# Optimization experiments

Measured on AMD Instinct MI355X. Metric: run time of the kernel, lower is better.

Reference implementation:

```python
import jax, jax.numpy as jnp
import numpy as np

# canonical 3x3 lattice offsets, (dy,dx) pairs in row-major kernel order (mmcv offset layout)
CANON = jnp.array([[-1,-1],[-1,0],[-1,1],[0,-1],[0,0],[0,1],[1,-1],[1,0],[1,1]], dtype=jnp.float32)  # (9,2)
BASE_DILATION = 1.0

def conv3x3(x, w, b):
    # x: (B,Cin,H,W), w: (Cout,Cin,3,3), stride 1, pad 1
    y = jax.lax.conv_general_dilated(x, w, window_strides=(1, 1), padding=((1, 1), (1, 1)),
                                     dimension_numbers=('NCHW', 'OIHW', 'NCHW'))
    return y + b[None, :, None, None]

def _bilinear_sample(img, ys, xs):
    # img: (Cg,H,W); ys,xs: (9,H,W) float sample coords. Zero outside bounds (per-corner).
    Cg, Hn, Wn = img.shape
    y0 = jnp.floor(ys); x0 = jnp.floor(xs)
    wy = ys - y0; wx = xs - x0
    y0i = y0.astype(jnp.int32); x0i = x0.astype(jnp.int32)
    flat = img.reshape(Cg, Hn * Wn)
    def corner(yi, xi, w):
        valid = (yi >= 0) & (yi < Hn) & (xi >= 0) & (xi < Wn)
        idx = jnp.clip(yi, 0, Hn - 1) * Wn + jnp.clip(xi, 0, Wn - 1)
        v = jnp.take(flat, idx.reshape(-1), axis=1).reshape((Cg,) + yi.shape)
        return v * (w * valid.astype(img.dtype))[None]
    return (corner(y0i, x0i, (1 - wy) * (1 - wx)) + corner(y0i, x0i + 1, (1 - wy) * wx)
            + corner(y0i + 1, x0i, wy * (1 - wx)) + corner(y0i + 1, x0i + 1, wy * wx))  # (Cg,9,H,W)

def setup_inputs() -> dict:
    key = jax.random.key(0)
    ks = jax.random.split(key, 7)
    B, C, H, W = 4, 256, 64, 64
    O, dg = 256, 1
    x = jax.random.normal(ks[0], (B, C, H, W), dtype=jnp.float32)
    weight = jax.random.normal(ks[1], (O, C, 3, 3), dtype=jnp.float32) * (2.0 / (C * 9)) ** 0.5
    bias = jnp.zeros((O,), dtype=jnp.float32)
    w_scale = jax.random.normal(ks[2], (dg, C, 3, 3), dtype=jnp.float32) * 0.01
    b_scale = jnp.full((dg,), 0.5, dtype=jnp.float32)
    w_mask = jax.random.normal(ks[3], (dg * 9, C, 3, 3), dtype=jnp.float32) * 0.01
    b_mask = jnp.zeros((dg * 9,), dtype=jnp.float32)
    return {"x": x, "weight": weight, "bias": bias, "w_scale": w_scale,
            "b_scale": b_scale, "w_mask": w_mask, "b_mask": b_mask}

def reference(x, weight, bias, w_scale, b_scale, w_mask, b_mask):
    B, C, H, W = x.shape
    dg = w_scale.shape[0]
    O = weight.shape[0]
    Cg = C // dg
    # radial scale s(x) >= 0 (use_zero_dilation=False): (B,dg,H,W)
    scale = jax.nn.relu(conv3x3(x, w_scale, b_scale)) * BASE_DILATION
    # modulation mask: (B,dg,9,H,W)
    mask = jax.nn.sigmoid(conv3x3(x, w_mask, b_mask)).reshape(B, dg, 9, H, W)
    # learned offset = scale * canonical lattice: (B,dg,9,2,H,W)
    off = scale[:, :, None, None, :, :] * CANON[None, None, :, :, None, None]
    # sampling coords: p0 (out pos * stride - pad) + kernel offset * dilation(=1) + learned offset
    base_y = jnp.arange(H, dtype=x.dtype)[None, None, None, :, None] - 1.0  # pad=1
    base_x = jnp.arange(W, dtype=x.dtype)[None, None, None, None, :] - 1.0
    ys = base_y + CANON[:, 0][None, None, :, None, None] + off[:, :, :, 0]  # (B,dg,9,H,W)
    xs = base_x + CANON[:, 1][None, None, :, None, None] + off[:, :, :, 1]
    xg = x.reshape(B, dg, Cg, H, W)
    sampled = jax.vmap(jax.vmap(_bilinear_sample))(xg, ys, xs)  # (B,dg,Cg,9,H,W)
    val = (sampled * mask[:, :, None]).reshape(B, C, 9, H, W)
    out = jnp.einsum('bckhw,ock->bohw', val, weight.reshape(O, C, 9))
    return out + bias[None, :, None, None]
```

## Files before the change

kernel.cpp:

```cpp
#include <hip/hip_runtime.h>
#include <stdint.h>

#define B_ 4
#define C_ 256
#define H_ 64
#define W_ 64
#define O_ 256
#define K_ 2304
#define HW 4096
#define NPIX 16384

typedef unsigned short u16;
typedef __attribute__((ext_vector_type(8))) short bf16x8;
typedef __attribute__((ext_vector_type(4))) float f32x4;

__device__ __forceinline__ u16 f2bf(float f) {
    union { float f; uint32_t u; } v; v.f = f;
    uint32_t u = v.u;
    return (u16)((u + 0x7FFFu + ((u >> 16) & 1u)) >> 16);
}
__device__ __forceinline__ float bf2f(u16 u) {
    union { uint32_t u; float f; } v; v.u = ((uint32_t)u) << 16;
    return v.f;
}

__global__ __launch_bounds__(512) void k_scale_mask(
    const float* __restrict__ x, const float* __restrict__ w_scale,
    const float* __restrict__ w_mask, float* __restrict__ part,
    u16* __restrict__ xT)
{
    __shared__ f32x4 wsm4[64 * 24];
    __shared__ float red[10 * 8 * 64];
    __shared__ u16 xt[64 * 72];

    int bh = blockIdx.x;
    int cg = blockIdx.y;
    int b = bh >> 6, h = bh & 63;
    int tid = threadIdx.x;
    int w = tid & 63;
    int wv = tid >> 6;

    float* wsm = (float*)wsm4;
    for (int i = tid; i < 64 * 96; i += 512) {
        int cl = i / 96, r = i % 96;
        int c = cg * 64 + cl;
        float v = 0.f;
        if (r < 9) {
            v = w_scale[c * 9 + r];
        } else if (r < 90) {
            int j = (r - 9) / 9, k = (r - 9) % 9;
            v = w_mask[((size_t)(j * C_ + c)) * 9 + k];
        }
        wsm[i] = v;
    }
    __syncthreads();

    float acc[10];
#pragma unroll
    for (int o = 0; o < 10; ++o) acc[o] = 0.f;

    const float* xb = x + (size_t)b * (C_ * HW);
#pragma unroll 1
    for (int cc = 0; cc < 8; ++cc) {
        int cl = wv * 8 + cc;
        const float* xp = xb + (cg * 64 + cl) * HW;
        float xv[9];
#pragma unroll
        for (int dy = -1; dy <= 1; ++dy) {
            int hh = h + dy;
            bool hv = (hh >= 0) && (hh < 64);
#pragma unroll
            for (int dx = -1; dx <= 1; ++dx) {
                int ww = w + dx;
                bool vld = hv && (ww >= 0) && (ww < 64);
                xv[(dy + 1) * 3 + (dx + 1)] = vld ? xp[hh * 64 + ww] : 0.f;
            }
        }
        xt[w * 72 + cl] = f2bf(xv[4]);

        const f32x4* wr4 = wsm4 + cl * 24;
        f32x4 wq[23];
#pragma unroll
        for (int q = 0; q < 23; ++q) wq[q] = wr4[q];

#pragma unroll
        for (int k = 0; k < 9; ++k)
            acc[0] = fmaf(xv[k], wq[k >> 2][k & 3], acc[0]);
#pragma unroll
        for (int j = 0; j < 9; ++j) {
#pragma unroll
            for (int k = 0; k < 9; ++k) {
                int r = 9 + j * 9 + k;
                acc[1 + j] = fmaf(xv[k], wq[r >> 2][r & 3], acc[1 + j]);
            }
        }
    }

#pragma unroll
    for (int o = 0; o < 10; ++o) red[(o * 8 + wv) * 64 + w] = acc[o];
    __syncthreads();

    {
        int ww = tid >> 3, c8 = (tid & 7) * 8;
        uint4 v = *(const uint4*)(xt + ww * 72 + c8);
        *(uint4*)(xT + ((size_t)(bh * 64 + ww)) * 256 + cg * 64 + c8) = v;
    }

    if (tid < 64) {
        float* pout = part + ((size_t)(cg * 256 + bh) * 10) * 64 + tid;
#pragma unroll
        for (int o = 0; o < 10; ++o) {
            float t = 0.f;
#pragma unroll
            for (int g = 0; g < 8; ++g) t += red[(o * 8 + g) * 64 + tid];
            pout[o * 64] = t;
        }
    }
}

__global__ __launch_bounds__(256) void k_finalize(
    const float* __restrict__ part, const float* __restrict__ b_scale,
    const float* __restrict__ b_mask, float* __restrict__ scale_o,
    float* __restrict__ mask_o)
{
    int tid = threadIdx.x;
    int bh = blockIdx.x * 4 + (tid >> 6);
    int w = tid & 63;
    int b = bh >> 6, h = bh & 63;
#pragma unroll
    for (int o = 0; o < 10; ++o) {
        float t = 0.f;
#pragma unroll
        for (int cg = 0; cg < 4; ++cg)
            t += part[((size_t)(cg * 256 + bh) * 10 + o) * 64 + w];
        if (o == 0) {
            float s = t + b_scale[0];
            scale_o[bh * 64 + w] = s > 0.f ? s : 0.f;
        } else {
            float m = t + b_mask[o - 1];
            mask_o[(b * 9 + (o - 1)) * HW + h * 64 + w] = 1.f / (1.f + expf(-m));
        }
    }
}

__global__ __launch_bounds__(256) void k_pack_w(const float* __restrict__ wgt,
                                                u16* __restrict__ wbf)
{
    int k = blockIdx.x, o = blockIdx.y, c = threadIdx.x;
    wbf[(size_t)o * K_ + k * 256 + c] = f2bf(wgt[(size_t)o * K_ + c * 9 + k]);
}

__global__ __launch_bounds__(256) void k_val2(
    const u16* __restrict__ xT, const float* __restrict__ scale_i,
    const float* __restrict__ mask_i, u16* __restrict__ val)
{
    int wv = threadIdx.x >> 6, lane = threadIdx.x & 63;
    int p = blockIdx.x * 4 + wv;
    int b = p >> 12, hw = p & 4095;
    int h = hw >> 6, w = hw & 63;
    float d = 1.f + scale_i[p];
    const u16* xb = xT + ((size_t)(b << 12)) * 256;
    u16* vout = val + (size_t)p * K_;
    int c0 = lane * 4;

#pragma unroll 3
    for (int k = 0; k < 9; ++k) {
        int dy = k / 3 - 1, dx = k % 3 - 1;
        float ysf = (float)(h - 1) + (float)dy * d;
        float xsf = (float)(w - 1) + (float)dx * d;
        float y0f = floorf(ysf), x0f = floorf(xsf);
        float wy = ysf - y0f, wx = xsf - x0f;
        int y0 = (int)y0f, x0 = (int)x0f;
        int y1 = y0 + 1, x1 = x0 + 1;
        float vy0 = (y0 >= 0 && y0 < 64) ? 1.f : 0.f;
        float vy1 = (y1 >= 0 && y1 < 64) ? 1.f : 0.f;
        float vx0 = (x0 >= 0 && x0 < 64) ? 1.f : 0.f;
        float vx1 = (x1 >= 0 && x1 < 64) ? 1.f : 0.f;

        float m = mask_i[(b * 9 + k) * HW + hw];
        float w00 = (1.f - wy) * (1.f - wx) * m * vy0 * vx0;
        float w01 = (1.f - wy) * wx * m * vy0 * vx1;
        float w10 = wy * (1.f - wx) * m * vy1 * vx0;
        float w11 = wy * wx * m * vy1 * vx1;

        int cy0 = min(max(y0, 0), 63), cy1 = min(max(y1, 0), 63);
        int cx0 = min(max(x0, 0), 63), cx1 = min(max(x1, 0), 63);

        const u16* p00 = xb + (size_t)(cy0 * 64 + cx0) * 256 + c0;
        const u16* p01 = xb + (size_t)(cy0 * 64 + cx1) * 256 + c0;
        const u16* p10 = xb + (size_t)(cy1 * 64 + cx0) * 256 + c0;
        const u16* p11 = xb + (size_t)(cy1 * 64 + cx1) * 256 + c0;
        ushort4 v00 = *(const ushort4*)p00;
        ushort4 v01 = *(const ushort4*)p01;
        ushort4 v10 = *(const ushort4*)p10;
        ushort4 v11 = *(const ushort4*)p11;

        float rx = fmaf(w00, bf2f(v00.x), fmaf(w01, bf2f(v01.x), fmaf(w10, bf2f(v10.x), w11 * bf2f(v11.x))));
        float ry = fmaf(w00, bf2f(v00.y), fmaf(w01, bf2f(v01.y), fmaf(w10, bf2f(v10.y), w11 * bf2f(v11.y))));
        float rz = fmaf(w00, bf2f(v00.z), fmaf(w01, bf2f(v01.z), fmaf(w10, bf2f(v10.z), w11 * bf2f(v11.z))));
        float rw = fmaf(w00, bf2f(v00.w), fmaf(w01, bf2f(v01.w), fmaf(w10, bf2f(v10.w), w11 * bf2f(v11.w))));

        ushort4 pk;
        pk.x = f2bf(rx); pk.y = f2bf(ry); pk.z = f2bf(rz); pk.w = f2bf(rw);
        *(ushort4*)(vout + k * 256 + c0) = pk;
    }
}

__global__ __launch_bounds__(256, 2) void k_gemm(
    const u16* __restrict__ wbf, const u16* __restrict__ val,
    const float* __restrict__ bias, float* __restrict__ out)
{
    __shared__ u16 As[128 * 72];
    __shared__ u16 Bs[64 * 72];
    int tid = threadIdx.x;
    int lane = tid & 63;
    int wv = tid >> 6;
    int wm = wv >> 1, wn = wv & 1;
    int n0 = blockIdx.x * 64;
    int m0 = blockIdx.y * 128;
    int l15 = lane & 15, l4 = lane >> 4;

    f32x4 acc[4][2];
#pragma unroll
    for (int i = 0; i < 4; ++i)
#pragma unroll
        for (int j = 0; j < 2; ++j) acc[i][j] = (f32x4){0.f, 0.f, 0.f, 0.f};

    int rr = tid >> 3;
    int c8 = (tid & 7) * 8;

    const u16* ap = wbf + (size_t)(m0 + rr) * K_ + c8;
    const u16* bp = val + (size_t)(n0 + rr) * K_ + c8;

    uint4 ra0 = *(const uint4*)(ap);
    uint4 ra1 = *(const uint4*)(ap + (size_t)32 * K_);
    uint4 ra2 = *(const uint4*)(ap + (size_t)64 * K_);
    uint4 ra3 = *(const uint4*)(ap + (size_t)96 * K_);
    uint4 rb0 = *(const uint4*)(bp);
    uint4 rb1 = *(const uint4*)(bp + (size_t)32 * K_);

    for (int k0 = 0; k0 < K_; k0 += 64) {
        __syncthreads();
        *(uint4*)(As + rr * 72 + c8) = ra0;
        *(uint4*)(As + (rr + 32) * 72 + c8) = ra1;
        *(uint4*)(As + (rr + 64) * 72 + c8) = ra2;
        *(uint4*)(As + (rr + 96) * 72 + c8) = ra3;
        *(uint4*)(Bs + rr * 72 + c8) = rb0;
        *(uint4*)(Bs + (rr + 32) * 72 + c8) = rb1;
        __syncthreads();

        int kn = k0 + 64;
        if (kn < K_) {
            ra0 = *(const uint4*)(ap + kn);
            ra1 = *(const uint4*)(ap + (size_t)32 * K_ + kn);
            ra2 = *(const uint4*)(ap + (size_t)64 * K_ + kn);
            ra3 = *(const uint4*)(ap + (size_t)96 * K_ + kn);
            rb0 = *(const uint4*)(bp + kn);
            rb1 = *(const uint4*)(bp + (size_t)32 * K_ + kn);
        }

#pragma unroll
        for (int kk = 0; kk < 2; ++kk) {
            bf16x8 af[4], bg[2];
#pragma unroll
            for (int i = 0; i < 4; ++i)
                af[i] = *(const bf16x8*)(As + (wm * 64 + i * 16 + l15) * 72 + kk * 32 + l4 * 8);
#pragma unroll
            for (int j = 0; j < 2; ++j)
                bg[j] = *(const bf16x8*)(Bs + (wn * 32 + j * 16 + l15) * 72 + kk * 32 + l4 * 8);
#pragma unroll
            for (int i = 0; i < 4; ++i)
#pragma unroll
                for (int j = 0; j < 2; ++j)
                    acc[i][j] = __builtin_amdgcn_mfma_f32_16x16x32_bf16(af[i], bg[j], acc[i][j], 0, 0, 0);
        }
    }

    int bidx = n0 >> 12;
    int hwbase = n0 & 4095;
#pragma unroll
    for (int i = 0; i < 4; ++i)
#pragma unroll
        for (int j = 0; j < 2; ++j)
#pragma unroll
            for (int t = 0; t < 4; ++t) {
                int row = wm * 64 + i * 16 + l4 * 4 + t;
                int col = wn * 32 + j * 16 + l15;
                int o = m0 + row;
                out[((size_t)(bidx * O_ + o)) * HW + hwbase + col] = acc[i][j][t] + bias[o];
            }
}

extern "C" void kernel_launch(void* const* d_in, const int* in_sizes, int n_in,
                              void* d_out, int out_size, void* d_ws, size_t ws_size,
                              hipStream_t stream) {
    const float* x       = (const float*)d_in[0];
    const float* weight  = (const float*)d_in[1];
    const float* bias    = (const float*)d_in[2];
    const float* w_scale = (const float*)d_in[3];
    const float* b_scale = (const float*)d_in[4];
    const float* w_mask  = (const float*)d_in[5];
    const float* b_mask  = (const float*)d_in[6];
    float* out = (float*)d_out;

    char* ws = (char*)d_ws;
    float* scale_ws = (float*)ws;
    float* mask_ws  = (float*)(ws + 65536);
    u16*   wbf      = (u16*)(ws + 65536 + 589824);
    u16*   val      = (u16*)(ws + 65536 + 589824 + 1179648);
    u16*   xT       = (u16*)(ws + 65536 + 589824 + 1179648 + 75497472);
    float* part_ws  = (float*)val;

    k_scale_mask<<<dim3(B_ * H_, 4), 512, 0, stream>>>(x, w_scale, w_mask, part_ws, xT);
    k_finalize<<<dim3(64), 256, 0, stream>>>(part_ws, b_scale, b_mask, scale_ws, mask_ws);
    k_pack_w<<<dim3(9, O_), 256, 0, stream>>>(weight, wbf);
    k_val2<<<dim3(NPIX / 4), 256, 0, stream>>>(xT, scale_ws, mask_ws, val);
    k_gemm<<<dim3(NPIX / 64, O_ / 128), 256, 0, stream>>>(wbf, val, bias, out);
}
```

Baseline: 171.2 us.

## Fuse deformable bilinear sampling into the GEMM B-tile load

Removes the separate k_val2 kernel that materialized the sampled/masked im2col matrix (about 75MB bf16) and instead computes the bilinear samples directly while loading each B tile in the GEMM. This avoids writing and re-reading the large intermediate buffer. In exchange, sampling is recomputed for each of the two M-blocks. The register prefetch of the next tile is dropped, so global load latency is no longer overlapped with the MFMA work.

```diff
diff --git a/kernel.cpp b/kernel.cpp
--- a/kernel.cpp
+++ b/kernel.cpp
@@ -19,9 +19,11 @@
     uint32_t u = v.u;
     return (u16)((u + 0x7FFFu + ((u >> 16) & 1u)) >> 16);
 }
-__device__ __forceinline__ float bf2f(u16 u) {
-    union { uint32_t u; float f; } v; v.u = ((uint32_t)u) << 16;
-    return v.f;
+__device__ __forceinline__ float bflo(uint32_t u) {
+    union { uint32_t u; float f; } v; v.u = u << 16; return v.f;
+}
+__device__ __forceinline__ float bfhi(uint32_t u) {
+    union { uint32_t u; float f; } v; v.u = u & 0xffff0000u; return v.f;
 }
 
 __global__ __launch_bounds__(512) void k_scale_mask(
@@ -150,64 +152,58 @@
     wbf[(size_t)o * K_ + k * 256 + c] = f2bf(wgt[(size_t)o * K_ + c * 9 + k]);
 }
 
-__global__ __launch_bounds__(256) void k_val2(
-    const u16* __restrict__ xT, const float* __restrict__ scale_i,
-    const float* __restrict__ mask_i, u16* __restrict__ val)
-{
-    int wv = threadIdx.x >> 6, lane = threadIdx.x & 63;
-    int p = blockIdx.x * 4 + wv;
-    int b = p >> 12, hw = p & 4095;
-    int h = hw >> 6, w = hw & 63;
-    float d = 1.f + scale_i[p];
-    const u16* xb = xT + ((size_t)(b << 12)) * 256;
-    u16* vout = val + (size_t)p * K_;
-    int c0 = lane * 4;
-
-#pragma unroll 3
-    for (int k = 0; k < 9; ++k) {
-        int dy = k / 3 - 1, dx = k % 3 - 1;
-        float ysf = (float)(h - 1) + (float)dy * d;
-        float xsf = (float)(w - 1) + (float)dx * d;
-        float y0f = floorf(ysf), x0f = floorf(xsf);
-        float wy = ysf - y0f, wx = xsf - x0f;
-        int y0 = (int)y0f, x0 = (int)x0f;
-        int y1 = y0 + 1, x1 = x0 + 1;
-        float vy0 = (y0 >= 0 && y0 < 64) ? 1.f : 0.f;
-        float vy1 = (y1 >= 0 && y1 < 64) ? 1.f : 0.f;
-        float vx0 = (x0 >= 0 && x0 < 64) ? 1.f : 0.f;
-        float vx1 = (x1 >= 0 && x1 < 64) ? 1.f : 0.f;
-
-        float m = mask_i[(b * 9 + k) * HW + hw];
-        float w00 = (1.f - wy) * (1.f - wx) * m * vy0 * vx0;
-        float w01 = (1.f - wy) * wx * m * vy0 * vx1;
-        float w10 = wy * (1.f - wx) * m * vy1 * vx0;
-        float w11 = wy * wx * m * vy1 * vx1;
-
-        int cy0 = min(max(y0, 0), 63), cy1 = min(max(y1, 0), 63);
-        int cx0 = min(max(x0, 0), 63), cx1 = min(max(x1, 0), 63);
-
-        const u16* p00 = xb + (size_t)(cy0 * 64 + cx0) * 256 + c0;
-        const u16* p01 = xb + (size_t)(cy0 * 64 + cx1) * 256 + c0;
-        const u16* p10 = xb + (size_t)(cy1 * 64 + cx0) * 256 + c0;
-        const u16* p11 = xb + (size_t)(cy1 * 64 + cx1) * 256 + c0;
-        ushort4 v00 = *(const ushort4*)p00;
-        ushort4 v01 = *(const ushort4*)p01;
-        ushort4 v10 = *(const ushort4*)p10;
-        ushort4 v11 = *(const ushort4*)p11;
-
-        float rx = fmaf(w00, bf2f(v00.x), fmaf(w01, bf2f(v01.x), fmaf(w10, bf2f(v10.x), w11 * bf2f(v11.x))));
-        float ry = fmaf(w00, bf2f(v00.y), fmaf(w01, bf2f(v01.y), fmaf(w10, bf2f(v10.y), w11 * bf2f(v11.y))));
-        float rz = fmaf(w00, bf2f(v00.z), fmaf(w01, bf2f(v01.z), fmaf(w10, bf2f(v10.z), w11 * bf2f(v11.z))));
-        float rw = fmaf(w00, bf2f(v00.w), fmaf(w01, bf2f(v01.w), fmaf(w10, bf2f(v10.w), w11 * bf2f(v11.w))));
-
-        ushort4 pk;
-        pk.x = f2bf(rx); pk.y = f2bf(ry); pk.z = f2bf(rz); pk.w = f2bf(rw);
-        *(ushort4*)(vout + k * 256 + c0) = pk;
-    }
-}
-
-__global__ __launch_bounds__(256, 2) void k_gemm(
-    const u16* __restrict__ wbf, const u16* __restrict__ val,
+__device__ __forceinline__ uint4 bilin8(const u16* __restrict__ xb, int cb,
+    int i00, int i01, int i10, int i11,
+    float w00, float w01, float w10, float w11)
+{
+    uint4 u00 = *(const uint4*)(xb + (size_t)i00 * 256 + cb);
+    uint4 u01 = *(const uint4*)(xb + (size_t)i01 * 256 + cb);
+    uint4 u10 = *(const uint4*)(xb + (size_t)i10 * 256 + cb);
+    uint4 u11 = *(const uint4*)(xb + (size_t)i11 * 256 + cb);
+    const uint32_t* p00 = &u00.x;
+    const uint32_t* p01 = &u01.x;
+    const uint32_t* p10 = &u10.x;
+    const uint32_t* p11 = &u11.x;
+    uint4 r;
+    uint32_t* pr = &r.x;
+#pragma unroll
+    for (int i = 0; i < 4; ++i) {
+        float lo = fmaf(w00, bflo(p00[i]), fmaf(w01, bflo(p01[i]),
+                   fmaf(w10, bflo(p10[i]), w11 * bflo(p11[i]))));
+        float hi = fmaf(w00, bfhi(p00[i]), fmaf(w01, bfhi(p01[i]),
+                   fmaf(w10, bfhi(p10[i]), w11 * bfhi(p11[i]))));
+        pr[i] = (uint32_t)f2bf(lo) | ((uint32_t)f2bf(hi) << 16);
+    }
+    return r;
+}
+
+__device__ __forceinline__ void tapcoord(int h, int w, float d, float mm,
+    int dy, int dx, float& w00, float& w01, float& w10, float& w11,
+    int& i00, int& i01, int& i10, int& i11)
+{
+    float ys = (float)(h - 1) + (float)dy * d;
+    float xs = (float)(w - 1) + (float)dx * d;
+    float y0f = floorf(ys), x0f = floorf(xs);
+    float wy = ys - y0f, wx = xs - x0f;
+    int y0 = (int)y0f, x0 = (int)x0f;
+    int y1 = y0 + 1, x1 = x0 + 1;
+    float vy0 = (y0 >= 0 && y0 < 64) ? 1.f : 0.f;
+    float vy1 = (y1 >= 0 && y1 < 64) ? 1.f : 0.f;
+    float vx0 = (x0 >= 0 && x0 < 64) ? 1.f : 0.f;
+    float vx1 = (x1 >= 0 && x1 < 64) ? 1.f : 0.f;
+    w00 = (1.f - wy) * (1.f - wx) * mm * vy0 * vx0;
+    w01 = (1.f - wy) * wx * mm * vy0 * vx1;
+    w10 = wy * (1.f - wx) * mm * vy1 * vx0;
+    w11 = wy * wx * mm * vy1 * vx1;
+    int cy0 = min(max(y0, 0), 63), cy1 = min(max(y1, 0), 63);
+    int cx0 = min(max(x0, 0), 63), cx1 = min(max(x1, 0), 63);
+    i00 = cy0 * 64 + cx0; i01 = cy0 * 64 + cx1;
+    i10 = cy1 * 64 + cx0; i11 = cy1 * 64 + cx1;
+}
+
+__global__ __launch_bounds__(256, 2) void k_gemm_fused(
+    const u16* __restrict__ wbf, const u16* __restrict__ xT,
+    const float* __restrict__ scale_i, const float* __restrict__ mask_i,
     const float* __restrict__ bias, float* __restrict__ out)
 {
     __shared__ u16 As[128 * 72];
@@ -229,35 +225,50 @@
     int rr = tid >> 3;
     int c8 = (tid & 7) * 8;
 
+    int b = n0 >> 12;
+    int hw0 = (n0 & 4095) + rr;
+    int hw1 = hw0 + 32;
+    int h0 = hw0 >> 6, w0c = hw0 & 63;
+    int h1 = hw1 >> 6, w1c = hw1 & 63;
+    float d0 = 1.f + scale_i[n0 + rr];
+    float d1 = 1.f + scale_i[n0 + rr + 32];
+    const u16* xb = xT + (((size_t)b) << 12) * 256;
+    const float* mrow = mask_i + (size_t)b * 9 * HW;
+
     const u16* ap = wbf + (size_t)(m0 + rr) * K_ + c8;
-    const u16* bp = val + (size_t)(n0 + rr) * K_ + c8;
-
-    uint4 ra0 = *(const uint4*)(ap);
-    uint4 ra1 = *(const uint4*)(ap + (size_t)32 * K_);
-    uint4 ra2 = *(const uint4*)(ap + (size_t)64 * K_);
-    uint4 ra3 = *(const uint4*)(ap + (size_t)96 * K_);
-    uint4 rb0 = *(const uint4*)(bp);
-    uint4 rb1 = *(const uint4*)(bp + (size_t)32 * K_);
+
+    float w00a, w01a, w10a, w11a, w00b, w01b, w10b, w11b;
+    int i00a, i01a, i10a, i11a, i00b, i01b, i10b, i11b;
 
     for (int k0 = 0; k0 < K_; k0 += 64) {
+        int tap = k0 >> 8;
+        if ((k0 & 255) == 0) {
+            int dy = tap / 3 - 1, dx = tap % 3 - 1;
+            float mm0 = mrow[tap * HW + hw0];
+            float mm1 = mrow[tap * HW + hw1];
+            tapcoord(h0, w0c, d0, mm0, dy, dx, w00a, w01a, w10a, w11a,
+                     i00a, i01a, i10a, i11a);
+            tapcoord(h1, w1c, d1, mm1, dy, dx, w00b, w01b, w10b, w11b,
+                     i00b, i01b, i10b, i11b);
+        }
+        int cb = (k0 & 255) + c8;
+
+        uint4 a0 = *(const uint4*)(ap + k0);
+        uint4 a1 = *(const uint4*)(ap + (size_t)32 * K_ + k0);
+        uint4 a2 = *(const uint4*)(ap + (size_t)64 * K_ + k0);
+        uint4 a3 = *(const uint4*)(ap + (size_t)96 * K_ + k0);
+
+        uint4 r0 = bilin8(xb, cb, i00a, i01a, i10a, i11a, w00a, w01a, w10a, w11a);
+        uint4 r1 = bilin8(xb, cb, i00b, i01b, i10b, i11b, w00b, w01b, w10b, w11b);
+
         __syncthreads();
-        *(uint4*)(As + rr * 72 + c8) = ra0;
-        *(uint4*)(As + (rr + 32) * 72 + c8) = ra1;
-        *(uint4*)(As + (rr + 64) * 72 + c8) = ra2;
-        *(uint4*)(As + (rr + 96) * 72 + c8) = ra3;
-        *(uint4*)(Bs + rr * 72 + c8) = rb0;
-        *(uint4*)(Bs + (rr + 32) * 72 + c8) = rb1;
+        *(uint4*)(As + rr * 72 + c8) = a0;
+        *(uint4*)(As + (rr + 32) * 72 + c8) = a1;
+        *(uint4*)(As + (rr + 64) * 72 + c8) = a2;
+        *(uint4*)(As + (rr + 96) * 72 + c8) = a3;
+        *(uint4*)(Bs + rr * 72 + c8) = r0;
+        *(uint4*)(Bs + (rr + 32) * 72 + c8) = r1;
         __syncthreads();
-
-        int kn = k0 + 64;
-        if (kn < K_) {
-            ra0 = *(const uint4*)(ap + kn);
-            ra1 = *(const uint4*)(ap + (size_t)32 * K_ + kn);
-            ra2 = *(const uint4*)(ap + (size_t)64 * K_ + kn);
-            ra3 = *(const uint4*)(ap + (size_t)96 * K_ + kn);
-            rb0 = *(const uint4*)(bp + kn);
-            rb1 = *(const uint4*)(bp + (size_t)32 * K_ + kn);
-        }
 
 #pragma unroll
         for (int kk = 0; kk < 2; ++kk) {
@@ -276,7 +287,6 @@
         }
     }
 
-    int bidx = n0 >> 12;
     int hwbase = n0 & 4095;
 #pragma unroll
     for (int i = 0; i < 4; ++i)
@@ -287,7 +297,7 @@
                 int row = wm * 64 + i * 16 + l4 * 4 + t;
                 int col = wn * 32 + j * 16 + l15;
                 int o = m0 + row;
-                out[((size_t)(bidx * O_ + o)) * HW + hwbase + col] = acc[i][j][t] + bias[o];
+                out[((size_t)(b * O_ + o)) * HW + hwbase + col] = acc[i][j][t] + bias[o];
             }
 }
 
@@ -307,13 +317,12 @@
     float* scale_ws = (float*)ws;
     float* mask_ws  = (float*)(ws + 65536);
     u16*   wbf      = (u16*)(ws + 65536 + 589824);
-    u16*   val      = (u16*)(ws + 65536 + 589824 + 1179648);
+    float* part_ws  = (float*)(ws + 65536 + 589824 + 1179648);
     u16*   xT       = (u16*)(ws + 65536 + 589824 + 1179648 + 75497472);
-    float* part_ws  = (float*)val;
 
     k_scale_mask<<<dim3(B_ * H_, 4), 512, 0, stream>>>(x, w_scale, w_mask, part_ws, xT);
     k_finalize<<<dim3(64), 256, 0, stream>>>(part_ws, b_scale, b_mask, scale_ws, mask_ws);
     k_pack_w<<<dim3(9, O_), 256, 0, stream>>>(weight, wbf);
-    k_val2<<<dim3(NPIX / 4), 256, 0, stream>>>(xT, scale_ws, mask_ws, val);
-    k_gemm<<<dim3(NPIX / 64, O_ / 128), 256, 0, stream>>>(wbf, val, bias, out);
-}
+    k_gemm_fused<<<dim3(NPIX / 64, O_ / 128), 256, 0, stream>>>(wbf, xT, scale_ws,
+                                                                mask_ws, bias, out);
+}
```

Result: faster. 165.2 us (-3.5%).
